# Optimization experiments

Measured on AMD Instinct MI355X. Metric: run time of the kernel, lower is better.

The kernel has to match this reference:

```python
import jax, jax.numpy as jnp
import numpy as np

N, F, H, T = 100000, 128, 128, 10
E = 1600000
NUM_GRAPHS = 512
BN_EPS = 1e-5


def setup_inputs() -> dict:
    key = jax.random.key(0)
    ks = jax.random.split(key, 16)
    x = jax.random.normal(ks[0], (N, F), dtype=jnp.float32)
    edge_index = jax.random.randint(ks[1], (2, E), 0, N, dtype=jnp.int64)
    batch = jnp.sort(jax.random.randint(ks[2], (N,), 0, NUM_GRAPHS, dtype=jnp.int64))
    s = lambda fin: 1.0 / np.sqrt(fin)
    return {
        "x": x, "edge_index": edge_index, "batch": batch,
        # GINConv 1 MLP: Linear(F,H) -> BN(H) -> ReLU -> Linear(H,H)
        "W1a": jax.random.uniform(ks[3], (F, H), jnp.float32, -s(F), s(F)),
        "b1a": jax.random.uniform(ks[4], (H,), jnp.float32, -s(F), s(F)),
        "g1": jnp.ones((H,), jnp.float32),
        "bt1": jnp.zeros((H,), jnp.float32),
        "W1b": jax.random.uniform(ks[5], (H, H), jnp.float32, -s(H), s(H)),
        "b1b": jax.random.uniform(ks[6], (H,), jnp.float32, -s(H), s(H)),
        # GINConv 2 MLP
        "W2a": jax.random.uniform(ks[7], (H, H), jnp.float32, -s(H), s(H)),
        "b2a": jax.random.uniform(ks[8], (H,), jnp.float32, -s(H), s(H)),
        "g2": jnp.ones((H,), jnp.float32),
        "bt2": jnp.zeros((H,), jnp.float32),
        "W2b": jax.random.uniform(ks[9], (H, H), jnp.float32, -s(H), s(H)),
        "b2b": jax.random.uniform(ks[10], (H,), jnp.float32, -s(H), s(H)),
        # final Linear(H, T)
        "Wl": jax.random.uniform(ks[11], (H, T), jnp.float32, -s(H), s(H)),
        "bl": jax.random.uniform(ks[12], (T,), jnp.float32, -s(H), s(H)),
    }


def _batchnorm(h, gamma, beta):
    # training-mode BN over the node dimension (biased variance), eps=1e-5
    mean = jnp.mean(h, axis=0)
    var = jnp.mean(jnp.square(h - mean), axis=0)
    return (h - mean) * jax.lax.rsqrt(var + BN_EPS) * gamma + beta


def _gin_conv(x, edge_index, Wa, ba, gamma, beta, Wb, bb):
    src, dst = edge_index[0], edge_index[1]
    # sum-aggregate neighbor messages: scatter-add x[src] into dst rows
    agg = jax.ops.segment_sum(x[src], dst, num_segments=x.shape[0])
    h = (x + agg) @ Wa + ba          # eps=0 in GINConv default
    h = jax.nn.relu(_batchnorm(h, gamma, beta))
    return h @ Wb + bb


def reference(x, edge_index, batch, W1a, b1a, g1, bt1, W1b, b1b,
              W2a, b2a, g2, bt2, W2b, b2b, Wl, bl):
    h = jax.nn.relu(_gin_conv(x, edge_index, W1a, b1a, g1, bt1, W1b, b1b))
    h = jax.nn.relu(_gin_conv(h, edge_index, W2a, b2a, g2, bt2, W2b, b2b))
    pooled = jax.ops.segment_sum(h, batch, num_segments=NUM_GRAPHS)  # [G, H]
    return pooled @ Wl + bl  # [G, T]
```

## Files before the change

kernel.cpp:

```cpp
#include <hip/hip_runtime.h>
#include <cstdint>
#include <cstddef>

#define NFEAT 128
#define TGRAPH 10
#define NGRAPHS 512
#define BN_EPS 1e-5f
#define BIN_CHUNK 2048

typedef __attribute__((ext_vector_type(8))) short bf16x8;
typedef __attribute__((ext_vector_type(4))) float f32x4;

__device__ __forceinline__ float bf2f(short s) {
    union { unsigned u; float f; } c;
    c.u = ((unsigned)(unsigned short)s) << 16;
    return c.f;
}
__device__ __forceinline__ short f2bf(float f) {
    union { float f; unsigned u; } c;
    c.f = f;
    unsigned u = c.u;
    return (short)((u + 0x7fffu + ((u >> 16) & 1u)) >> 16);
}
__device__ __forceinline__ void acc2(float& a, float& b, unsigned v) {
    union { unsigned u; float f; } lo, hi;
    lo.u = v << 16;
    hi.u = v & 0xffff0000u;
    a += lo.f;
    b += hi.f;
}


__global__ __launch_bounds__(256) void k_bucket_hist(const int* __restrict__ dst,
                                                     int* __restrict__ bhist, int E) {
    __shared__ int h[256];
    int t = threadIdx.x;
    h[t] = 0;
    __syncthreads();
    for (int e = blockIdx.x * blockDim.x + t; e < E; e += gridDim.x * blockDim.x)
        atomicAdd(&h[dst[e] >> 9], 1);
    __syncthreads();
    if (h[t]) atomicAdd(&bhist[t], h[t]);
}

__global__ void k_bucket_scan(const int* __restrict__ bhist, int* __restrict__ bbase,
                              int* __restrict__ cur256, int E) {
    __shared__ int s[256];
    int t = threadIdx.x;
    int v = bhist[t];
    s[t] = v;
    __syncthreads();
    for (int off = 1; off < 256; off <<= 1) {
        int x = 0;
        if (t >= off) x = s[t - off];
        __syncthreads();
        if (t >= off) s[t] += x;
        __syncthreads();
    }
    int excl = s[t] - v;
    bbase[t] = excl;
    cur256[t] = excl;
    if (t == 255) bbase[256] = E;
}

__global__ __launch_bounds__(256) void k_bin_scatter(const int* __restrict__ src,
                                                     const int* __restrict__ dst,
                                                     int* __restrict__ cur256,
                                                     int2* __restrict__ binned, int E) {
    __shared__ int hist[256];
    __shared__ int base[256];
    int t = threadIdx.x;
    int e0 = blockIdx.x * BIN_CHUNK;
    int e1 = min(e0 + BIN_CHUNK, E);
    hist[t] = 0;
    __syncthreads();
    for (int e = e0 + t; e < e1; e += 256) {
        int b = dst[e] >> 9;
        atomicAdd(&hist[b], 1);
    }
    __syncthreads();
    int c = hist[t];
    if (c > 0) base[t] = atomicAdd(&cur256[t], c);
    __syncthreads();
    hist[t] = 0;
    __syncthreads();
    for (int e = e0 + t; e < e1; e += 256) {
        int d = dst[e];
        int b = d >> 9;
        int loc = atomicAdd(&hist[b], 1);
        binned[base[b] + loc] = make_int2(src[e], d);
    }
}

__global__ __launch_bounds__(512) void k_bucket_csr(const int2* __restrict__ binned,
                                                    const int* __restrict__ bbase,
                                                    int* __restrict__ rowptr,
                                                    int* __restrict__ adj,
                                                    int N, int E, int nb) {
    __shared__ int deg[512];
    __shared__ int cur[512];
    int b = blockIdx.x;
    int t = threadIdx.x;
    int e0 = bbase[b], e1 = bbase[b + 1];
    deg[t] = 0;
    __syncthreads();
    for (int e = e0 + t; e < e1; e += 512)
        atomicAdd(&deg[binned[e].y & 511], 1);
    __syncthreads();
    int v = deg[t];
    for (int off = 1; off < 512; off <<= 1) {
        int x = 0;
        if (t >= off) x = deg[t - off];
        __syncthreads();
        if (t >= off) deg[t] += x;
        __syncthreads();
    }
    int excl = deg[t] - v;
    cur[t] = excl;
    int node = b * 512 + t;
    if (node < N) rowptr[node] = e0 + excl;
    if (b == nb - 1 && t == 0) rowptr[N] = E;
    __syncthreads();
    for (int e = e0 + t; e < e1; e += 512) {
        int2 p = binned[e];
        int loc = atomicAdd(&cur[p.y & 511], 1);
        adj[e0 + loc] = p.x;
    }
}

__global__ void k_prep(const float* __restrict__ x, short* __restrict__ xbf,
                       const float* __restrict__ W0, const float* __restrict__ W1,
                       const float* __restrict__ W2, const float* __restrict__ W3,
                       short* __restrict__ Wf, int n4) {
    int i = blockIdx.x * blockDim.x + threadIdx.x;
    if (i < n4) {
        float4 v = ((const float4*)x)[i];
        ushort4 o;
        o.x = (unsigned short)f2bf(v.x);
        o.y = (unsigned short)f2bf(v.y);
        o.z = (unsigned short)f2bf(v.z);
        o.w = (unsigned short)f2bf(v.w);
        ((ushort4*)xbf)[i] = o;
    } else {
        int idx = i - n4;
        if (idx < 4 * 16384) {
            int w = idx >> 14, r = idx & 16383;
            int j = r & 7, lane = (r >> 3) & 63, ct = (r >> 9) & 7, kc = r >> 12;
            int k = kc * 32 + (lane >> 4) * 8 + j;
            int n = ct * 16 + (lane & 15);
            const float* W = (w == 0) ? W0 : (w == 1) ? W1 : (w == 2) ? W2 : W3;
            Wf[idx] = f2bf(W[k * NFEAT + n]);
        }
    }
}

__global__ __launch_bounds__(256) void k_aggregate_v4(const short* __restrict__ X,
                                                      const int* __restrict__ rowptr,
                                                      const int* __restrict__ adj,
                                                      short* __restrict__ XA, int N) {
    int tid = threadIdx.x;
    int lane = tid & 63;
    int g = lane >> 4;
    int p = lane & 15;
    int wid = (blockIdx.x * blockDim.x + tid) >> 6;
    if (wid >= N) return;
    const uint4* Xv = (const uint4*)X;
    float acc[8];
#pragma unroll
    for (int j = 0; j < 8; j++) acc[j] = 0.f;
    int r0 = rowptr[wid], r1 = rowptr[wid + 1];
    for (int e = r0; e < r1; e += 8) {
        int e0 = e + g, e1 = e + 4 + g;
        uint4 v0 = {0u, 0u, 0u, 0u}, v1 = {0u, 0u, 0u, 0u};
        if (e0 < r1) v0 = Xv[(size_t)adj[e0] * 16 + p];
        if (e1 < r1) v1 = Xv[(size_t)adj[e1] * 16 + p];
        acc2(acc[0], acc[1], v0.x);
        acc2(acc[2], acc[3], v0.y);
        acc2(acc[4], acc[5], v0.z);
        acc2(acc[6], acc[7], v0.w);
        acc2(acc[0], acc[1], v1.x);
        acc2(acc[2], acc[3], v1.y);
        acc2(acc[4], acc[5], v1.z);
        acc2(acc[6], acc[7], v1.w);
    }
#pragma unroll
    for (int j = 0; j < 8; j++) {
        acc[j] += __shfl_xor(acc[j], 16);
        acc[j] += __shfl_xor(acc[j], 32);
    }
    if (g == 0) {
        uint4 sv = Xv[(size_t)wid * 16 + p];
        acc2(acc[0], acc[1], sv.x);
        acc2(acc[2], acc[3], sv.y);
        acc2(acc[4], acc[5], sv.z);
        acc2(acc[6], acc[7], sv.w);
        uint4 o;
        o.x = (unsigned)(unsigned short)f2bf(acc[0]) | ((unsigned)(unsigned short)f2bf(acc[1]) << 16);
        o.y = (unsigned)(unsigned short)f2bf(acc[2]) | ((unsigned)(unsigned short)f2bf(acc[3]) << 16);
        o.z = (unsigned)(unsigned short)f2bf(acc[4]) | ((unsigned)(unsigned short)f2bf(acc[5]) << 16);
        o.w = (unsigned)(unsigned short)f2bf(acc[6]) | ((unsigned)(unsigned short)f2bf(acc[7]) << 16);
        size_t dst = ((size_t)(wid >> 4) * 4 + (p >> 2)) * 512 +
                     (size_t)(((p & 3) * 16 + (wid & 15)) * 8);
        *(uint4*)(XA + dst) = o;
    }
}

template <bool BN_RELU_IN, bool RELU_OUT, bool STATS, bool FRAG_OUT>
__global__ __launch_bounds__(256) void k_gemm_mfma(const short* __restrict__ A,
                                                   const short* __restrict__ Wf,
                                                   const float* __restrict__ bias,
                                                   float* __restrict__ stats,
                                                   const float* __restrict__ gamma,
                                                   const float* __restrict__ beta,
                                                   short* __restrict__ C, int N) {
    __shared__ float s_aux[256];
    __shared__ short c_tile[4][512];
    int tid = threadIdx.x;
    int wave = tid >> 6, lane = tid & 63;
    int quad = lane >> 4, l16 = lane & 15;
    int row_base = blockIdx.x * 128 + wave * 32;

    if constexpr (STATS) {
        s_aux[tid] = 0.f;
        __syncthreads();
    }
    if constexpr (BN_RELU_IN) {
        if (tid < NFEAT) {
            float mean = stats[tid] / (float)N;
            float var = stats[NFEAT + tid] / (float)N - mean * mean;
            float inv = rsqrtf(var + BN_EPS);
            float sc = gamma[tid] * inv;
            s_aux[tid] = sc;
            s_aux[NFEAT + tid] = beta[tid] - mean * sc;
        }
        __syncthreads();
    }

    f32x4 acc[2][8];
#pragma unroll
    for (int i = 0; i < 2; i++)
#pragma unroll
        for (int j = 0; j < 8; j++) acc[i][j] = (f32x4){0.f, 0.f, 0.f, 0.f};

    const short* af = A + ((size_t)(blockIdx.x * 8 + wave * 2) * 4) * 512;

#pragma unroll
    for (int kc = 0; kc < 4; ++kc) {
        bf16x8 a0 = *(const bf16x8*)(af + (size_t)kc * 512 + lane * 8);
        bf16x8 a1 = *(const bf16x8*)(af + (size_t)(4 + kc) * 512 + lane * 8);
        if constexpr (BN_RELU_IN) {
            int koff = kc * 32 + quad * 8;
#pragma unroll
            for (int j = 0; j < 8; j++) {
                float sc = s_aux[koff + j];
                float sh = s_aux[NFEAT + koff + j];
                a0[j] = f2bf(fmaxf(bf2f(a0[j]) * sc + sh, 0.f));
                a1[j] = f2bf(fmaxf(bf2f(a1[j]) * sc + sh, 0.f));
            }
        }
        const short* wp = Wf + ((size_t)(kc * 8) * 64 + lane) * 8;
#pragma unroll
        for (int ct = 0; ct < 8; ++ct) {
            bf16x8 b = *(const bf16x8*)(wp + (size_t)ct * 64 * 8);
            acc[0][ct] = __builtin_amdgcn_mfma_f32_16x16x32_bf16(a0, b, acc[0][ct], 0, 0, 0);
            acc[1][ct] = __builtin_amdgcn_mfma_f32_16x16x32_bf16(a1, b, acc[1][ct], 0, 0, 0);
        }
    }

    short* tile = &c_tile[wave][0];
    int row2 = lane >> 1, half = lane & 1;
#pragma unroll
    for (int ct = 0; ct < 8; ++ct) {
        int col = ct * 16 + l16;
        float bv = bias[col];
        float ls = 0.f, ls2 = 0.f;
#pragma unroll
        for (int rt = 0; rt < 2; ++rt) {
#pragma unroll
            for (int reg = 0; reg < 4; ++reg) {
                int lrow = rt * 16 + quad * 4 + reg;
                float v = acc[rt][ct][reg] + bv;
                if constexpr (RELU_OUT) v = fmaxf(v, 0.f);
                if constexpr (STATS) {
                    if (row_base + lrow < N) { ls += v; ls2 += v * v; }
                }
                tile[lrow * 16 + l16] = f2bf(v);
            }
        }
        if constexpr (STATS) {
            atomicAdd(&s_aux[col], ls);
            atomicAdd(&s_aux[NFEAT + col], ls2);
        }
        uint4 val = *(const uint4*)(tile + row2 * 16 + half * 8);
        int grow = row_base + row2;
        if (grow < N) {
            int col0 = ct * 16 + half * 8;
            if constexpr (FRAG_OUT) {
                size_t addr = ((size_t)(grow >> 4) * 4 + (col0 >> 5)) * 512 +
                              (size_t)((((col0 >> 3) & 3) * 16 + (grow & 15)) * 8);
                *(uint4*)(C + addr) = val;
            } else {
                *(uint4*)(C + (size_t)grow * NFEAT + col0) = val;
            }
        }
    }

    if constexpr (STATS) {
        __syncthreads();
        if (tid < NFEAT) {
            atomicAdd(&stats[tid], s_aux[tid]);
            atomicAdd(&stats[NFEAT + tid], s_aux[NFEAT + tid]);
        }
    }
}

__global__ __launch_bounds__(256) void k_pool2(const short* __restrict__ H2,
                                               const int* __restrict__ batch,
                                               float* __restrict__ pooled, int N) {
    int t = threadIdx.x;
    int c2 = t & 63;
    int rofs = t >> 6;
    int n0 = blockIdx.x * 128;
    int cur = -1;
    float ax = 0.f, ay = 0.f;
    for (int i = 0; i < 32; ++i) {
        int n = n0 + rofs + i * 4;
        if (n >= N) break;
        int g = batch[n];
        if (g != cur) {
            if (cur >= 0) {
                atomicAdd(&pooled[cur * NFEAT + c2 * 2], ax);
                atomicAdd(&pooled[cur * NFEAT + c2 * 2 + 1], ay);
            }
            cur = g; ax = 0.f; ay = 0.f;
        }
        unsigned v = *(const unsigned*)(H2 + (size_t)n * NFEAT + c2 * 2);
        ax += bf2f((short)(v & 0xffff));
        ay += bf2f((short)(v >> 16));
    }
    if (cur >= 0) {
        atomicAdd(&pooled[cur * NFEAT + c2 * 2], ax);
        atomicAdd(&pooled[cur * NFEAT + c2 * 2 + 1], ay);
    }
}

__global__ void k_final(const float* __restrict__ pooled, const float* __restrict__ Wl,
                        const float* __restrict__ bl, float* __restrict__ out) {
    int idx = blockIdx.x * blockDim.x + threadIdx.x;
    if (idx >= NGRAPHS * TGRAPH) return;
    int g = idx / TGRAPH, t = idx % TGRAPH;
    const float* p = pooled + (size_t)g * NFEAT;
    float acc = bl[t];
#pragma unroll 16
    for (int k = 0; k < NFEAT; ++k) acc += p[k] * Wl[k * TGRAPH + t];
    out[idx] = acc;
}

extern "C" void kernel_launch(void* const* d_in, const int* in_sizes, int n_in,
                              void* d_out, int out_size, void* d_ws, size_t ws_size,
                              hipStream_t stream) {
    const float* x = (const float*)d_in[0];
    const int* ei = (const int*)d_in[1];
    const int* batch = (const int*)d_in[2];
    const float* W1a = (const float*)d_in[3];
    const float* b1a = (const float*)d_in[4];
    const float* g1 = (const float*)d_in[5];
    const float* bt1 = (const float*)d_in[6];
    const float* W1b = (const float*)d_in[7];
    const float* b1b = (const float*)d_in[8];
    const float* W2a = (const float*)d_in[9];
    const float* b2a = (const float*)d_in[10];
    const float* g2 = (const float*)d_in[11];
    const float* bt2 = (const float*)d_in[12];
    const float* W2b = (const float*)d_in[13];
    const float* b2b = (const float*)d_in[14];
    const float* Wl = (const float*)d_in[15];
    const float* bl = (const float*)d_in[16];
    float* out = (float*)d_out;

    int N = in_sizes[2];
    int E = in_sizes[1] / 2;
    int nb = (N + 511) >> 9;
    const int* src = ei;
    const int* dst = ei + E;

    int gemmBlocks = (N + 127) / 128;
    int padRows = gemmBlocks * 128;

    char* ws = (char*)d_ws;
    size_t off = 0;
    auto alloc = [&](size_t bytes) -> void* {
        void* p = ws + off;
        off = (off + bytes + 255) & ~(size_t)255;
        return p;
    };
    short* xbf = (short*)alloc((size_t)N * NFEAT * 2);
    short* ag = (short*)alloc((size_t)padRows * NFEAT * 2);
    short* ybf = (short*)alloc((size_t)padRows * NFEAT * 2);
    short* hbf = (short*)alloc((size_t)N * NFEAT * 2);
    short* h2bf = (short*)alloc((size_t)N * NFEAT * 2);
    short* Wf = (short*)alloc((size_t)4 * 16384 * 2);
    int* adj = (int*)alloc((size_t)E * 4);
    int2* binned = (int2*)alloc((size_t)E * 8);
    int* rowptr = (int*)alloc((size_t)(N + 1) * 4);
    int* bbase = (int*)alloc(257 * 4);
    int* cur256 = (int*)alloc(256 * 4);
    int* bhist = (int*)alloc(256 * 4);
    float* stats1 = (float*)alloc(256 * 4);
    float* stats2 = (float*)alloc(256 * 4);
    float* pooled = (float*)alloc((size_t)NGRAPHS * NFEAT * 4);
    size_t zbytes = (char*)(pooled + (size_t)NGRAPHS * NFEAT) - (char*)bhist;

    hipMemsetAsync(bhist, 0, zbytes, stream);

    k_bucket_hist<<<784, 256, 0, stream>>>(dst, bhist, E);
    k_bucket_scan<<<1, 256, 0, stream>>>(bhist, bbase, cur256, E);
    k_bin_scatter<<<(E + BIN_CHUNK - 1) / BIN_CHUNK, 256, 0, stream>>>(src, dst, cur256, binned, E);
    k_bucket_csr<<<nb, 512, 0, stream>>>(binned, bbase, rowptr, adj, N, E, nb);

    int n4 = N * NFEAT / 4;
    int prepTot = n4 + 4 * 16384;
    k_prep<<<(prepTot + 255) / 256, 256, 0, stream>>>(x, xbf, W1a, W1b, W2a, W2b, Wf, n4);

    int aggBlocks = (N + 3) / 4;

    k_aggregate_v4<<<aggBlocks, 256, 0, stream>>>(xbf, rowptr, adj, ag, N);
    k_gemm_mfma<false, false, true, true><<<gemmBlocks, 256, 0, stream>>>(
        ag, Wf + 0 * 16384, b1a, stats1, nullptr, nullptr, ybf, N);
    k_gemm_mfma<true, true, false, false><<<gemmBlocks, 256, 0, stream>>>(
        ybf, Wf + 1 * 16384, b1b, stats1, g1, bt1, hbf, N);

    k_aggregate_v4<<<aggBlocks, 256, 0, stream>>>(hbf, rowptr, adj, ag, N);
    k_gemm_mfma<false, false, true, true><<<gemmBlocks, 256, 0, stream>>>(
        ag, Wf + 2 * 16384, b2a, stats2, nullptr, nullptr, ybf, N);
    k_gemm_mfma<true, true, false, false><<<gemmBlocks, 256, 0, stream>>>(
        ybf, Wf + 3 * 16384, b2b, stats2, g2, bt2, h2bf, N);

    k_pool2<<<(N + 127) / 128, 256, 0, stream>>>(h2bf, batch, pooled, N);
    k_final<<<(NGRAPHS * TGRAPH + 255) / 256, 256, 0, stream>>>(pooled, Wl, bl, out);
}
```

Baseline: 490.2 us.

## Fuse graph pooling into final GEMM epilogue and unroll aggregation deeper

The last MLP GEMM now does the per-graph sum pooling in its epilogue through a small shared-memory buffer indexed relative to the block's first graph id. This removes the h2 bf16 write and the separate pool kernel. The aggregation loop now gathers four neighbour rows per iteration instead of two, giving more loads in flight. STATS partial sums are reduced across quads with shuffles before the shared atomics. The GSPAN=8 window assumes a 128-row block spans at most 8 consecutive graphs; the masking could alias graphs if sorted batches were sparser, though with about 195 nodes per graph this holds here.

```diff
diff --git a/kernel.cpp b/kernel.cpp
--- a/kernel.cpp
+++ b/kernel.cpp
@@ -7,6 +7,7 @@
 #define NGRAPHS 512
 #define BN_EPS 1e-5f
 #define BIN_CHUNK 2048
+#define GSPAN 8
 
 typedef __attribute__((ext_vector_type(8))) short bf16x8;
 typedef __attribute__((ext_vector_type(4))) float f32x4;
@@ -169,19 +170,22 @@
 #pragma unroll
     for (int j = 0; j < 8; j++) acc[j] = 0.f;
     int r0 = rowptr[wid], r1 = rowptr[wid + 1];
-    for (int e = r0; e < r1; e += 8) {
-        int e0 = e + g, e1 = e + 4 + g;
+    for (int e = r0; e < r1; e += 16) {
+        int ea = e + g, eb = e + 4 + g, ec = e + 8 + g, ed = e + 12 + g;
         uint4 v0 = {0u, 0u, 0u, 0u}, v1 = {0u, 0u, 0u, 0u};
-        if (e0 < r1) v0 = Xv[(size_t)adj[e0] * 16 + p];
-        if (e1 < r1) v1 = Xv[(size_t)adj[e1] * 16 + p];
-        acc2(acc[0], acc[1], v0.x);
-        acc2(acc[2], acc[3], v0.y);
-        acc2(acc[4], acc[5], v0.z);
-        acc2(acc[6], acc[7], v0.w);
-        acc2(acc[0], acc[1], v1.x);
-        acc2(acc[2], acc[3], v1.y);
-        acc2(acc[4], acc[5], v1.z);
-        acc2(acc[6], acc[7], v1.w);
+        uint4 v2 = {0u, 0u, 0u, 0u}, v3 = {0u, 0u, 0u, 0u};
+        if (ea < r1) v0 = Xv[(size_t)adj[ea] * 16 + p];
+        if (eb < r1) v1 = Xv[(size_t)adj[eb] * 16 + p];
+        if (ec < r1) v2 = Xv[(size_t)adj[ec] * 16 + p];
+        if (ed < r1) v3 = Xv[(size_t)adj[ed] * 16 + p];
+        acc2(acc[0], acc[1], v0.x); acc2(acc[2], acc[3], v0.y);
+        acc2(acc[4], acc[5], v0.z); acc2(acc[6], acc[7], v0.w);
+        acc2(acc[0], acc[1], v1.x); acc2(acc[2], acc[3], v1.y);
+        acc2(acc[4], acc[5], v1.z); acc2(acc[6], acc[7], v1.w);
+        acc2(acc[0], acc[1], v2.x); acc2(acc[2], acc[3], v2.y);
+        acc2(acc[4], acc[5], v2.z); acc2(acc[6], acc[7], v2.w);
+        acc2(acc[0], acc[1], v3.x); acc2(acc[2], acc[3], v3.y);
+        acc2(acc[4], acc[5], v3.z); acc2(acc[6], acc[7], v3.w);
     }
 #pragma unroll
     for (int j = 0; j < 8; j++) {
@@ -190,10 +194,8 @@
     }
     if (g == 0) {
         uint4 sv = Xv[(size_t)wid * 16 + p];
-        acc2(acc[0], acc[1], sv.x);
-        acc2(acc[2], acc[3], sv.y);
-        acc2(acc[4], acc[5], sv.z);
-        acc2(acc[6], acc[7], sv.w);
+        acc2(acc[0], acc[1], sv.x); acc2(acc[2], acc[3], sv.y);
+        acc2(acc[4], acc[5], sv.z); acc2(acc[6], acc[7], sv.w);
         uint4 o;
         o.x = (unsigned)(unsigned short)f2bf(acc[0]) | ((unsigned)(unsigned short)f2bf(acc[1]) << 16);
         o.y = (unsigned)(unsigned short)f2bf(acc[2]) | ((unsigned)(unsigned short)f2bf(acc[3]) << 16);
@@ -205,25 +207,31 @@
     }
 }
 
-template <bool BN_RELU_IN, bool RELU_OUT, bool STATS, bool FRAG_OUT>
+template <bool BN_RELU_IN, bool RELU_OUT, bool STATS, bool FRAG_OUT, bool POOL>
 __global__ __launch_bounds__(256) void k_gemm_mfma(const short* __restrict__ A,
                                                    const short* __restrict__ Wf,
                                                    const float* __restrict__ bias,
                                                    float* __restrict__ stats,
                                                    const float* __restrict__ gamma,
                                                    const float* __restrict__ beta,
+                                                   const int* __restrict__ batch,
+                                                   float* __restrict__ pooled,
                                                    short* __restrict__ C, int N) {
     __shared__ float s_aux[256];
     __shared__ short c_tile[4][512];
+    __shared__ float s_pool[GSPAN][NFEAT];
     int tid = threadIdx.x;
     int wave = tid >> 6, lane = tid & 63;
     int quad = lane >> 4, l16 = lane & 15;
     int row_base = blockIdx.x * 128 + wave * 32;
 
-    if constexpr (STATS) {
-        s_aux[tid] = 0.f;
-        __syncthreads();
-    }
+    int gbase = 0;
+    if constexpr (POOL) {
+        int first = blockIdx.x * 128;
+        gbase = (first < N) ? batch[first] : 0;
+        for (int i = tid; i < GSPAN * NFEAT; i += 256) s_pool[i >> 7][i & 127] = 0.f;
+    }
+    if constexpr (STATS) s_aux[tid] = 0.f;
     if constexpr (BN_RELU_IN) {
         if (tid < NFEAT) {
             float mean = stats[tid] / (float)N;
@@ -233,8 +241,8 @@
             s_aux[tid] = sc;
             s_aux[NFEAT + tid] = beta[tid] - mean * sc;
         }
-        __syncthreads();
-    }
+    }
+    if constexpr (STATS || BN_RELU_IN || POOL) __syncthreads();
 
     f32x4 acc[2][8];
 #pragma unroll
@@ -267,6 +275,17 @@
         }
     }
 
+    int dg[8];
+    if constexpr (POOL) {
+#pragma unroll
+        for (int rt = 0; rt < 2; ++rt)
+#pragma unroll
+            for (int reg = 0; reg < 4; ++reg) {
+                int row = row_base + rt * 16 + quad * 4 + reg;
+                dg[rt * 4 + reg] = (row < N) ? (batch[row] - gbase) : -1;
+            }
+    }
+
     short* tile = &c_tile[wave][0];
     int row2 = lane >> 1, half = lane & 1;
 #pragma unroll
@@ -274,6 +293,8 @@
         int col = ct * 16 + l16;
         float bv = bias[col];
         float ls = 0.f, ls2 = 0.f;
+        int cg = -1;
+        float ps = 0.f;
 #pragma unroll
         for (int rt = 0; rt < 2; ++rt) {
 #pragma unroll
@@ -284,23 +305,43 @@
                 if constexpr (STATS) {
                     if (row_base + lrow < N) { ls += v; ls2 += v * v; }
                 }
-                tile[lrow * 16 + l16] = f2bf(v);
-            }
+                if constexpr (POOL) {
+                    int d = dg[rt * 4 + reg];
+                    if (d != cg) {
+                        if (cg >= 0) atomicAdd(&s_pool[cg & (GSPAN - 1)][col], ps);
+                        cg = d; ps = 0.f;
+                    }
+                    if (d >= 0) ps += v;
+                } else {
+                    tile[lrow * 16 + l16] = f2bf(v);
+                }
+            }
+        }
+        if constexpr (POOL) {
+            if (cg >= 0) atomicAdd(&s_pool[cg & (GSPAN - 1)][col], ps);
         }
         if constexpr (STATS) {
-            atomicAdd(&s_aux[col], ls);
-            atomicAdd(&s_aux[NFEAT + col], ls2);
-        }
-        uint4 val = *(const uint4*)(tile + row2 * 16 + half * 8);
-        int grow = row_base + row2;
-        if (grow < N) {
-            int col0 = ct * 16 + half * 8;
-            if constexpr (FRAG_OUT) {
-                size_t addr = ((size_t)(grow >> 4) * 4 + (col0 >> 5)) * 512 +
-                              (size_t)((((col0 >> 3) & 3) * 16 + (grow & 15)) * 8);
-                *(uint4*)(C + addr) = val;
-            } else {
-                *(uint4*)(C + (size_t)grow * NFEAT + col0) = val;
+            ls += __shfl_xor(ls, 16);
+            ls += __shfl_xor(ls, 32);
+            ls2 += __shfl_xor(ls2, 16);
+            ls2 += __shfl_xor(ls2, 32);
+            if (quad == 0) {
+                atomicAdd(&s_aux[col], ls);
+                atomicAdd(&s_aux[NFEAT + col], ls2);
+            }
+        }
+        if constexpr (!POOL) {
+            uint4 val = *(const uint4*)(tile + row2 * 16 + half * 8);
+            int grow = row_base + row2;
+            if (grow < N) {
+                int col0 = ct * 16 + half * 8;
+                if constexpr (FRAG_OUT) {
+                    size_t addr = ((size_t)(grow >> 4) * 4 + (col0 >> 5)) * 512 +
+                                  (size_t)((((col0 >> 3) & 3) * 16 + (grow & 15)) * 8);
+                    *(uint4*)(C + addr) = val;
+                } else {
+                    *(uint4*)(C + (size_t)grow * NFEAT + col0) = val;
+                }
             }
         }
     }
@@ -312,35 +353,15 @@
             atomicAdd(&stats[NFEAT + tid], s_aux[NFEAT + tid]);
         }
     }
-}
-
-__global__ __launch_bounds__(256) void k_pool2(const short* __restrict__ H2,
-                                               const int* __restrict__ batch,
-                                               float* __restrict__ pooled, int N) {
-    int t = threadIdx.x;
-    int c2 = t & 63;
-    int rofs = t >> 6;
-    int n0 = blockIdx.x * 128;
-    int cur = -1;
-    float ax = 0.f, ay = 0.f;
-    for (int i = 0; i < 32; ++i) {
-        int n = n0 + rofs + i * 4;
-        if (n >= N) break;
-        int g = batch[n];
-        if (g != cur) {
-            if (cur >= 0) {
-                atomicAdd(&pooled[cur * NFEAT + c2 * 2], ax);
-                atomicAdd(&pooled[cur * NFEAT + c2 * 2 + 1], ay);
-            }
-            cur = g; ax = 0.f; ay = 0.f;
-        }
-        unsigned v = *(const unsigned*)(H2 + (size_t)n * NFEAT + c2 * 2);
-        ax += bf2f((short)(v & 0xffff));
-        ay += bf2f((short)(v >> 16));
-    }
-    if (cur >= 0) {
-        atomicAdd(&pooled[cur * NFEAT + c2 * 2], ax);
-        atomicAdd(&pooled[cur * NFEAT + c2 * 2 + 1], ay);
+    if constexpr (POOL) {
+        __syncthreads();
+        for (int i = tid; i < GSPAN * NFEAT; i += 256) {
+            float v = s_pool[i >> 7][i & 127];
+            if (v != 0.f) {
+                int gg = gbase + (i >> 7);
+                if (gg < NGRAPHS) atomicAdd(&pooled[gg * NFEAT + (i & 127)], v);
+            }
+        }
     }
 }
 
@@ -398,7 +419,6 @@
     short* ag = (short*)alloc((size_t)padRows * NFEAT * 2);
     short* ybf = (short*)alloc((size_t)padRows * NFEAT * 2);
     short* hbf = (short*)alloc((size_t)N * NFEAT * 2);
-    short* h2bf = (short*)alloc((size_t)N * NFEAT * 2);
     short* Wf = (short*)alloc((size_t)4 * 16384 * 2);
     int* adj = (int*)alloc((size_t)E * 4);
     int2* binned = (int2*)alloc((size_t)E * 8);
@@ -425,17 +445,16 @@
     int aggBlocks = (N + 3) / 4;
 
     k_aggregate_v4<<<aggBlocks, 256, 0, stream>>>(xbf, rowptr, adj, ag, N);
-    k_gemm_mfma<false, false, true, true><<<gemmBlocks, 256, 0, stream>>>(
-        ag, Wf + 0 * 16384, b1a, stats1, nullptr, nullptr, ybf, N);
-    k_gemm_mfma<true, true, false, false><<<gemmBlocks, 256, 0, stream>>>(
-        ybf, Wf + 1 * 16384, b1b, stats1, g1, bt1, hbf, N);
+    k_gemm_mfma<false, false, true, true, false><<<gemmBlocks, 256, 0, stream>>>(
+        ag, Wf + 0 * 16384, b1a, stats1, nullptr, nullptr, nullptr, nullptr, ybf, N);
+    k_gemm_mfma<true, true, false, false, false><<<gemmBlocks, 256, 0, stream>>>(
+        ybf, Wf + 1 * 16384, b1b, stats1, g1, bt1, nullptr, nullptr, hbf, N);
 
     k_aggregate_v4<<<aggBlocks, 256, 0, stream>>>(hbf, rowptr, adj, ag, N);
-    k_gemm_mfma<false, false, true, true><<<gemmBlocks, 256, 0, stream>>>(
-        ag, Wf + 2 * 16384, b2a, stats2, nullptr, nullptr, ybf, N);
-    k_gemm_mfma<true, true, false, false><<<gemmBlocks, 256, 0, stream>>>(
-        ybf, Wf + 3 * 16384, b2b, stats2, g2, bt2, h2bf, N);
-
-    k_pool2<<<(N + 127) / 128, 256, 0, stream>>>(h2bf, batch, pooled, N);
+    k_gemm_mfma<false, false, true, true, false><<<gemmBlocks, 256, 0, stream>>>(
+        ag, Wf + 2 * 16384, b2a, stats2, nullptr, nullptr, nullptr, nullptr, ybf, N);
+    k_gemm_mfma<true, true, false, false, true><<<gemmBlocks, 256, 0, stream>>>(
+        ybf, Wf + 3 * 16384, b2b, stats2, g2, bt2, batch, pooled, nullptr, N);
+
     k_final<<<(NGRAPHS * TGRAPH + 255) / 256, 256, 0, stream>>>(pooled, Wl, bl, out);
 }
```

Result: faster. 457.8 us (-6.6%).
